# Performance work log

Hardware: AMD Instinct MI355X
Metric: run time of the kernel (lower is better)

The kernel has to match this reference:

```python
import jax, jax.numpy as jnp
import numpy as np

N_NODES, N_EDGES, N_GRAPHS = 50000, 800000, 512
F_IN, HID, DIM_OUT = 128, 256, 16


def setup_inputs() -> dict:
    key = jax.random.key(0)
    ks = jax.random.split(key, 16)
    glorot = lambda k, fi, fo: jax.random.normal(k, (fi, fo), jnp.float32) * jnp.sqrt(2.0 / (fi + fo))
    return {
        "x": jax.random.normal(ks[0], (N_NODES, F_IN), jnp.float32),
        "edge_index": jax.random.randint(ks[1], (2, N_EDGES), 0, N_NODES, dtype=jnp.int32),
        "batch": jnp.sort(jax.random.randint(ks[2], (N_NODES,), 0, N_GRAPHS, dtype=jnp.int32)),
        "mol_wt": jax.random.uniform(ks[3], (N_GRAPHS, 1), jnp.float32),
        "n_rings": jax.random.uniform(ks[4], (N_GRAPHS, 1), jnp.float32),
        "W1": glorot(ks[5], F_IN, HID), "b1": jnp.zeros((HID,), jnp.float32),
        "W2": glorot(ks[6], HID, HID), "b2": jnp.zeros((HID,), jnp.float32),
        "W3": glorot(ks[7], HID, HID), "b3": jnp.zeros((HID,), jnp.float32),
        "fcW1": glorot(ks[8], HID + 2, 196), "fcb1": jnp.zeros((196,), jnp.float32),
        "fcW2": glorot(ks[9], 196, DIM_OUT), "fcb2": jnp.zeros((DIM_OUT,), jnp.float32),
    }


def _gcn_conv(x, W, b, src, dst, deg_inv_sqrt, n_nodes):
    # PyG GCNConv: linear transform, then D^-1/2 (A+I) D^-1/2 aggregation, then bias
    xw = x @ W  # [N, HID]
    norm = deg_inv_sqrt[src] * deg_inv_sqrt[dst]  # [E+N]
    msg = norm[:, None] * xw[src]  # gather + scale
    out = jax.ops.segment_sum(msg, dst, num_segments=n_nodes)  # scatter-add at targets
    return out + b


def reference(x, edge_index, batch, mol_wt, n_rings,
              W1, b1, W2, b2, W3, b3, fcW1, fcb1, fcW2, fcb2):
    n_nodes = x.shape[0]
    self_loop = jnp.arange(n_nodes, dtype=edge_index.dtype)
    src = jnp.concatenate([edge_index[0], self_loop])
    dst = jnp.concatenate([edge_index[1], self_loop])
    deg = jax.ops.segment_sum(jnp.ones_like(dst, dtype=x.dtype), dst, num_segments=n_nodes)
    deg_inv_sqrt = jnp.where(deg > 0, jax.lax.rsqrt(deg), 0.0)

    h = jax.nn.relu(_gcn_conv(x, W1, b1, src, dst, deg_inv_sqrt, n_nodes))
    h = jax.nn.relu(_gcn_conv(h, W2, b2, src, dst, deg_inv_sqrt, n_nodes))
    h = jax.nn.relu(_gcn_conv(h, W3, b3, src, dst, deg_inv_sqrt, n_nodes))

    n_graphs = mol_wt.shape[0]
    sums = jax.ops.segment_sum(h, batch, num_segments=n_graphs)
    counts = jax.ops.segment_sum(jnp.ones((n_nodes,), h.dtype), batch, num_segments=n_graphs)
    hg = sums / jnp.maximum(counts, 1.0)[:, None]  # global mean pool

    hg = jnp.concatenate([hg, mol_wt, n_rings], axis=1)  # [G, 258]
    hg = jax.nn.relu(hg @ fcW1 + fcb1)
    return hg @ fcW2 + fcb2
```

## Files before the change

kernel.cpp:

```cpp
#include <hip/hip_runtime.h>

#define NN 50000
#define NE 800000
#define NG 512
#define FIN 128
#define HID 256
#define NBUK 196
#define SEGSZ 2048

typedef short short8 __attribute__((ext_vector_type(8)));
typedef float f32x4 __attribute__((ext_vector_type(4)));
typedef float f32x2 __attribute__((ext_vector_type(2)));
typedef unsigned short u16x8 __attribute__((ext_vector_type(8)));
typedef unsigned int u32x2 __attribute__((ext_vector_type(2)));
typedef unsigned int u32x4 __attribute__((ext_vector_type(4)));

static inline int cdiv(int a, int b) { return (a + b - 1) / b; }

static __device__ inline unsigned short f2bf(float f) {
    unsigned int u = __float_as_uint(f);
    unsigned int r = (u + 0x7FFF + ((u >> 16) & 1)) >> 16;
    return (unsigned short)r;
}
static __device__ inline float bf2f(unsigned short h) {
    return __uint_as_float(((unsigned int)h) << 16);
}
static __device__ inline float bflo(unsigned int p) { return __uint_as_float(p << 16); }
static __device__ inline float bfhi(unsigned int p) { return __uint_as_float(p & 0xFFFF0000u); }

static __device__ __forceinline__ f32x2 pkadd(f32x2 a, f32x2 b) {
    f32x2 r;
    asm("v_pk_add_f32 %0, %1, %2" : "=v"(r) : "v"(a), "v"(b));
    return r;
}

template <int J>
static __device__ __forceinline__ int bswz(int v) {
    return __builtin_amdgcn_ds_swizzle(v, (J << 5) | 0x18);
}

typedef __attribute__((address_space(1))) unsigned int gu32;
typedef __attribute__((address_space(3))) unsigned int lu32;
static __device__ __forceinline__ void gload16(const unsigned short* g, unsigned short* l) {
    __builtin_amdgcn_global_load_lds((const gu32*)(const void*)g, (lu32*)(void*)l, 16, 0, 0);
}


__global__ __launch_bounds__(256) void hist_bucket_kernel(const int* __restrict__ dst,
                                                          int* __restrict__ gbuk) {
    __shared__ int lh[NBUK];
    int tid = threadIdx.x;
    for (int j = tid; j < NBUK; j += 256) lh[j] = 0;
    __syncthreads();
    int base = blockIdx.x * 2048;
    #pragma unroll
    for (int k = 0; k < 8; ++k) {
        int i = base + k * 256 + tid;
        if (i < NE) atomicAdd(&lh[dst[i] >> 8], 1);
    }
    __syncthreads();
    for (int j = tid; j < NBUK; j += 256) if (lh[j]) atomicAdd(&gbuk[j], lh[j]);
}

__global__ void goff_kernel(const int* __restrict__ batch, int* __restrict__ goff) {
    int i = blockIdx.x * 256 + threadIdx.x;
    if (i >= NN) return;
    int b = batch[i];
    int pb = (i == 0) ? -1 : batch[i - 1];
    for (int g = pb + 1; g <= b; ++g) goff[g] = i;
    if (i == NN - 1) for (int g = b + 1; g <= NG; ++g) goff[g] = NN;
}

__global__ void buk_scan_kernel(const int* __restrict__ gbuk, int* __restrict__ bukoff,
                                int* __restrict__ bukcur) {
    __shared__ int ws[4];
    int tid = threadIdx.x, lane = tid & 63, wid = tid >> 6;
    int v = (tid < NBUK) ? gbuk[tid] : 0;
    int incl = v;
    #pragma unroll
    for (int off = 1; off < 64; off <<= 1) {
        int u = __shfl_up(incl, off, 64);
        if (lane >= off) incl += u;
    }
    if (lane == 63) ws[wid] = incl;
    __syncthreads();
    int woff = 0;
    for (int w = 0; w < wid; ++w) woff += ws[w];
    int ex = woff + incl - v;
    if (tid < NBUK) { bukoff[tid] = ex; bukcur[tid] = ex; }
    if (tid == NBUK - 1) bukoff[NBUK] = ex + v;
}

__global__ __launch_bounds__(256) void scatter_kernel(const int* __restrict__ src,
                                                      const int* __restrict__ dst,
                                                      int* __restrict__ bukcur,
                                                      unsigned int* __restrict__ pairs) {
    __shared__ int lh[NBUK];
    __shared__ int lbase[NBUK];
    int tid = threadIdx.x;
    for (int j = tid; j < NBUK; j += 256) lh[j] = 0;
    __syncthreads();
    int base = blockIdx.x * 2048;
    int d[8], s[8];
    #pragma unroll
    for (int k = 0; k < 8; ++k) {
        int i = base + k * 256 + tid;
        if (i < NE) {
            d[k] = dst[i]; s[k] = src[i];
            atomicAdd(&lh[d[k] >> 8], 1);
        } else d[k] = -1;
    }
    __syncthreads();
    for (int j = tid; j < NBUK; j += 256) lbase[j] = lh[j] ? atomicAdd(&bukcur[j], lh[j]) : 0;
    __syncthreads();
    for (int j = tid; j < NBUK; j += 256) lh[j] = 0;
    __syncthreads();
    #pragma unroll
    for (int k = 0; k < 8; ++k) {
        if (d[k] >= 0) {
            int b = d[k] >> 8;
            int loc = atomicAdd(&lh[b], 1);
            pairs[lbase[b] + loc] = ((unsigned int)s[k] << 16) | (unsigned int)(d[k] & 255);
        }
    }
}

__global__ __launch_bounds__(256) void local_csr_kernel(const unsigned int* __restrict__ pairs,
                                                        const int* __restrict__ bukoff,
                                                        int* __restrict__ row_ptr,
                                                        int* __restrict__ col8,
                                                        float* __restrict__ dis) {
    __shared__ int fcnt[256];
    __shared__ int foff[256];
    __shared__ int fws[4];
    int b = blockIdx.x, tid = threadIdx.x;
    int beg = bukoff[b], end = bukoff[b + 1];
    fcnt[tid] = 0;
    __syncthreads();
    for (int i = beg + tid; i < end; i += 256) atomicAdd(&fcnt[pairs[i] & 255], 1);
    __syncthreads();
    int lane = tid & 63, wid = tid >> 6;
    int v = fcnt[tid], incl = v;
    #pragma unroll
    for (int off = 1; off < 64; off <<= 1) {
        int u = __shfl_up(incl, off, 64);
        if (lane >= off) incl += u;
    }
    if (lane == 63) fws[wid] = incl;
    __syncthreads();
    int woff = 0;
    for (int w = 0; w < wid; ++w) woff += fws[w];
    int ex = woff + incl - v;
    foff[tid] = ex;
    int gid = b * 256 + tid;
    if (gid < NN) {
        row_ptr[gid] = beg + ex;
        dis[gid] = rsqrtf((float)v + 1.0f);
    }
    if (b == 0 && tid == 0) row_ptr[NN] = NE;
    __syncthreads();
    for (int i = beg + tid; i < end; i += 256) {
        unsigned int p = pairs[i];
        int loc = atomicAdd(&foff[p & 255], 1);
        col8[beg + loc] = (int)(p >> 16) << 3;
    }
}

__global__ __launch_bounds__(256) void segperm_kernel(const int* __restrict__ row_ptr,
                                                      const float* __restrict__ dis,
                                                      u32x4* __restrict__ desc) {
    __shared__ int hist[256];
    __shared__ int ws[4];
    int tid = threadIdx.x;
    int base = blockIdx.x * SEGSZ;
    int segN = NN - base; if (segN > SEGSZ) segN = SEGSZ;
    hist[tid] = 0;
    __syncthreads();
    int dbin[8], rb[8], dreal[8];
    #pragma unroll
    for (int k = 0; k < 8; ++k) {
        int j = k * 256 + tid;
        if (j < segN) {
            rb[k] = row_ptr[base + j];
            dreal[k] = row_ptr[base + j + 1] - rb[k];
            int d = dreal[k] > 255 ? 255 : dreal[k];
            dbin[k] = d;
            atomicAdd(&hist[d], 1);
        } else dbin[k] = -1;
    }
    __syncthreads();
    int lane = tid & 63, wid = tid >> 6;
    int v = hist[tid], incl = v;
    #pragma unroll
    for (int off = 1; off < 64; off <<= 1) {
        int u = __shfl_up(incl, off, 64);
        if (lane >= off) incl += u;
    }
    if (lane == 63) ws[wid] = incl;
    __syncthreads();
    int woff = 0;
    for (int w = 0; w < wid; ++w) woff += ws[w];
    __syncthreads();
    hist[tid] = woff + incl - v;
    __syncthreads();
    #pragma unroll
    for (int k = 0; k < 8; ++k) {
        if (dbin[k] >= 0) {
            int rank = atomicAdd(&hist[dbin[k]], 1);
            int node = base + k * 256 + tid;
            u32x4 dd;
            dd.x = (unsigned int)(node * 8);
            dd.y = (unsigned int)rb[k];
            dd.z = (unsigned int)(rb[k] + dreal[k]);
            dd.w = __float_as_uint(dis[node]);
            desc[base + rank] = dd;
        }
    }
}

__global__ void cast_scale_kernel(const float* __restrict__ x, const float* __restrict__ dis,
                                  unsigned short* __restrict__ Xb, int n4) {
    int i = blockIdx.x * 256 + threadIdx.x;
    if (i < n4) {
        int node = i >> 5;
        int f4 = i & 31;
        int s = f4 >> 3;
        int o = f4 & 7;
        float dv = dis[node];
        float4 v = ((const float4*)x)[i];
        ushort4 w;
        w.x = f2bf(dv * v.x); w.y = f2bf(dv * v.y); w.z = f2bf(dv * v.z); w.w = f2bf(dv * v.w);
        ((ushort4*)Xb)[((size_t)s * NN + (size_t)node) * 8 + o] = w;
    }
}

__global__ void tcast_all_kernel(const float* __restrict__ W1, const float* __restrict__ W2,
                                 const float* __restrict__ W3,
                                 unsigned short* __restrict__ W1t, unsigned short* __restrict__ W2t,
                                 unsigned short* __restrict__ W3t) {
    int idx = blockIdx.x * 256 + threadIdx.x;
    if (idx < FIN * 256) {
        int n = idx / FIN, k = idx - n * FIN;
        W1t[idx] = f2bf(W1[(size_t)k * 256 + n]);
    } else if (idx < FIN * 256 + HID * 256) {
        int t = idx - FIN * 256;
        int n = t / HID, k = t - n * HID;
        W2t[t] = f2bf(W2[(size_t)k * 256 + n]);
    } else {
        int t = idx - FIN * 256 - HID * 256;
        int n = t / HID, k = t - n * HID;
        W3t[t] = f2bf(W3[(size_t)k * 256 + n]);
    }
}

#define CLD 136
template <int MODE>
__global__ __launch_bounds__(256) void gemm128_kernel(
        const unsigned short* __restrict__ A, const unsigned short* __restrict__ Bt,
        const float* __restrict__ dis, const float* __restrict__ bias,
        unsigned short* __restrict__ Cout, int M, int K) {
    __shared__ unsigned short smem[128 * CLD];
    unsigned short* As = smem;
    unsigned short* Bs = smem + 4096;
    const int tid = threadIdx.x;
    const int bm = blockIdx.x * 128, bn = blockIdx.y * 128;
    const int wave = tid >> 6, lane = tid & 63;
    const int l16 = lane & 15, quad = lane >> 4;
    const int wm = (wave & 1) * 64, wn = (wave >> 1) * 64;

    int srow0 = tid >> 2, skc = (tid & 3) * 8;
    int srow1 = (256 + tid) >> 2;
    int ar0 = bm + srow0; if (ar0 > M - 1) ar0 = M - 1;
    int ar1 = bm + srow1; if (ar1 > M - 1) ar1 = M - 1;

    f32x4 acc[4][4];
    #pragma unroll
    for (int i = 0; i < 4; ++i)
        #pragma unroll
        for (int j = 0; j < 4; ++j) acc[i][j] = (f32x4){0.f, 0.f, 0.f, 0.f};

    for (int k0 = 0; k0 < K; k0 += 32) {
        gload16(A + (size_t)ar0 * K + k0 + skc, &As[(size_t)tid * 8]);
        gload16(A + (size_t)ar1 * K + k0 + skc, &As[(size_t)(256 + tid) * 8]);
        gload16(Bt + (size_t)(bn + srow0) * K + k0 + skc, &Bs[(size_t)tid * 8]);
        gload16(Bt + (size_t)(bn + srow1) * K + k0 + skc, &Bs[(size_t)(256 + tid) * 8]);
        __syncthreads();
        short8 af[4], bf[4];
        #pragma unroll
        for (int mt = 0; mt < 4; ++mt) af[mt] = *(const short8*)&As[(wm + mt * 16 + l16) * 32 + quad * 8];
        #pragma unroll
        for (int nt = 0; nt < 4; ++nt) bf[nt] = *(const short8*)&Bs[(wn + nt * 16 + l16) * 32 + quad * 8];
        #pragma unroll
        for (int mt = 0; mt < 4; ++mt)
            #pragma unroll
            for (int nt = 0; nt < 4; ++nt)
                acc[mt][nt] = __builtin_amdgcn_mfma_f32_16x16x32_bf16(af[mt], bf[nt], acc[mt][nt], 0, 0, 0);
        __syncthreads();
    }
    float bv[4];
    #pragma unroll
    for (int nt = 0; nt < 4; ++nt) bv[nt] = bias[bn + wn + nt * 16 + l16];
    #pragma unroll
    for (int mt = 0; mt < 4; ++mt) {
        #pragma unroll
        for (int r = 0; r < 4; ++r) {
            int lrow = wm + mt * 16 + quad * 4 + r;
            int grow = bm + lrow; if (grow > M - 1) grow = M - 1;
            float dv = (MODE == 0) ? dis[grow] : 1.0f;
            #pragma unroll
            for (int nt = 0; nt < 4; ++nt) {
                float v = fmaxf(acc[mt][nt][r] + bv[nt], 0.f);
                if (MODE == 0) v *= dv;
                smem[lrow * CLD + wn + nt * 16 + l16] = f2bf(v);
            }
        }
    }
    __syncthreads();
    for (int c = tid; c < 2048; c += 256) {
        int lrow = c >> 4, coff = (c & 15) << 3;
        int grow = bm + lrow;
        if (grow < M) {
            if (MODE == 0) {
                int gcol = bn + coff;
                int s = gcol >> 5, o = gcol & 31;
                *(u16x8*)(Cout + ((size_t)s * M + (size_t)grow) * 32 + o) =
                    *(const u16x8*)&smem[lrow * CLD + coff];
            } else {
                *(u16x8*)(Cout + (size_t)grow * HID + bn + coff) =
                    *(const u16x8*)&smem[lrow * CLD + coff];
            }
        }
    }
}
#undef CLD

template <int S>
__global__ __launch_bounds__(256) void agg_slice_kernel(
        const unsigned short* __restrict__ Hb, const u32x4* __restrict__ desc,
        const int* __restrict__ col8,
        unsigned short* __restrict__ Out, int n, int nchunk) {
    constexpr int LOGS = (S == 8) ? 3 : 2;
    int bid = blockIdx.x;
    int s = bid & (S - 1);
    int chunk = nchunk - 1 - (bid >> LOGS);
    int idx = chunk * 32 + (threadIdx.x >> 3);
    if (idx >= n) return;
    int lane8 = threadIdx.x & 7;
    u32x4 d = desc[idx];
    int node8 = (int)d.x;
    int e = (int)d.y, eend = (int)d.z;
    float dv = __uint_as_float(d.w);
    const u32x2* Hv = (const u32x2*)Hb + (size_t)s * NN * 8;
    u32x2 p = Hv[node8 + lane8];
    f32x2 a01 = {bflo(p.x), bfhi(p.x)};
    f32x2 a23 = {bflo(p.y), bfhi(p.y)};

    for (; e + 16 <= eend; e += 16) {
        int cv0 = col8[e + lane8];
        int cv1 = col8[e + 8 + lane8];
        u32x2 m[16];
#define G0(J) m[J] = Hv[bswz<J>(cv0) + lane8];
#define G1(J) m[8 + J] = Hv[bswz<J>(cv1) + lane8];
        G0(0) G0(1) G0(2) G0(3) G0(4) G0(5) G0(6) G0(7)
        G1(0) G1(1) G1(2) G1(3) G1(4) G1(5) G1(6) G1(7)
#undef G0
#undef G1
        #pragma unroll
        for (int j = 0; j < 16; ++j) {
            f32x2 lo = {bflo(m[j].x), bfhi(m[j].x)};
            f32x2 hi = {bflo(m[j].y), bfhi(m[j].y)};
            a01 = pkadd(a01, lo);
            a23 = pkadd(a23, hi);
        }
    }
    if (e + 8 <= eend) {
        int cv0 = col8[e + lane8];
        u32x2 m[8];
#define G0(J) m[J] = Hv[bswz<J>(cv0) + lane8];
        G0(0) G0(1) G0(2) G0(3) G0(4) G0(5) G0(6) G0(7)
#undef G0
        #pragma unroll
        for (int j = 0; j < 8; ++j) {
            f32x2 lo = {bflo(m[j].x), bfhi(m[j].x)};
            f32x2 hi = {bflo(m[j].y), bfhi(m[j].y)};
            a01 = pkadd(a01, lo);
            a23 = pkadd(a23, hi);
        }
        e += 8;
    }
    int t = eend - e;
    if (t > 0) {
        int il = e + lane8; if (il >= eend) il = eend - 1;
        int cv0 = col8[il];
        u32x2 m[7];
#define GT(J) if (J < t) m[J] = Hv[bswz<J>(cv0) + lane8];
        GT(0) GT(1) GT(2) GT(3) GT(4) GT(5) GT(6)
#undef GT
#define AT(J) if (J < t) { f32x2 lo = {bflo(m[J].x), bfhi(m[J].x)}; \
                           f32x2 hi = {bflo(m[J].y), bfhi(m[J].y)}; \
                           a01 = pkadd(a01, lo); a23 = pkadd(a23, hi); }
        AT(0) AT(1) AT(2) AT(3) AT(4) AT(5) AT(6)
#undef AT
    }
    int node = node8 >> 3;
    u32x2 o;
    o.x = (unsigned int)f2bf(dv * a01.x) | ((unsigned int)f2bf(dv * a01.y) << 16);
    o.y = (unsigned int)f2bf(dv * a23.x) | ((unsigned int)f2bf(dv * a23.y) << 16);
    __builtin_nontemporal_store(o, (u32x2*)Out + (size_t)node * (S * 8) + s * 8 + lane8);
}

__global__ __launch_bounds__(256) void pool_mlp_kernel(
        const unsigned short* __restrict__ H, const int* __restrict__ goff,
        const float* __restrict__ mol, const float* __restrict__ rings,
        const float* __restrict__ fcW1, const float* __restrict__ fcb1,
        const float* __restrict__ fcW2, const float* __restrict__ fcb2,
        float* __restrict__ out) {
    __shared__ float s_hg[258];
    __shared__ float s_t[196];
    int g = blockIdx.x, tid = threadIdx.x;
    int beg = goff[g], end = goff[g + 1];
    float acc = 0.f;
    for (int i = beg; i < end; ++i) acc += bf2f(H[(size_t)i * HID + tid]);
    s_hg[tid] = acc / fmaxf((float)(end - beg), 1.0f);
    if (tid == 0) { s_hg[256] = mol[g]; s_hg[257] = rings[g]; }
    __syncthreads();
    if (tid < 196) {
        float a = fcb1[tid];
        for (int k = 0; k < 258; ++k) a = fmaf(s_hg[k], fcW1[k * 196 + tid], a);
        s_t[tid] = fmaxf(a, 0.f);
    }
    __syncthreads();
    if (tid < 16) {
        float a = fcb2[tid];
        for (int k = 0; k < 196; ++k) a = fmaf(s_t[k], fcW2[k * 16 + tid], a);
        out[g * 16 + tid] = a;
    }
}

extern "C" void kernel_launch(void* const* d_in, const int* in_sizes, int n_in,
                              void* d_out, int out_size, void* d_ws, size_t ws_size,
                              hipStream_t stream) {
    const float* x     = (const float*)d_in[0];
    const int*   ei    = (const int*)d_in[1];
    const int*   batch = (const int*)d_in[2];
    const float* mol   = (const float*)d_in[3];
    const float* rings = (const float*)d_in[4];
    const float* W1 = (const float*)d_in[5];
    const float* b1 = (const float*)d_in[6];
    const float* W2 = (const float*)d_in[7];
    const float* b2 = (const float*)d_in[8];
    const float* W3 = (const float*)d_in[9];
    const float* b3 = (const float*)d_in[10];
    const float* fcW1 = (const float*)d_in[11];
    const float* fcb1 = (const float*)d_in[12];
    const float* fcW2 = (const float*)d_in[13];
    const float* fcb2 = (const float*)d_in[14];
    float* out = (float*)d_out;
    const int* src = ei;
    const int* dst = ei + NE;

    char* w = (char*)d_ws;
    auto alloc = [&](size_t bytes) {
        char* p = w;
        w += (bytes + 255) & ~(size_t)255;
        return p;
    };
    int*   gbuk    = (int*)alloc((size_t)NBUK * 4);
    int*   bukoff  = (int*)alloc((size_t)(NBUK + 1) * 4);
    int*   bukcur  = (int*)alloc((size_t)NBUK * 4);
    int*   row_ptr = (int*)alloc((size_t)(NN + 1) * 4);
    int*   goff    = (int*)alloc((size_t)(NG + 1) * 4);
    float* dis     = (float*)alloc((size_t)NN * 4);
    u32x4* desc    = (u32x4*)alloc((size_t)NN * 16);
    unsigned int* pairs = (unsigned int*)alloc((size_t)NE * 4);
    int*   col8    = (int*)alloc((size_t)NE * 4);
    unsigned short* Xs  = (unsigned short*)alloc((size_t)NN * FIN * 2);
    unsigned short* Xa  = (unsigned short*)alloc((size_t)NN * FIN * 2);
    unsigned short* Hs  = (unsigned short*)alloc((size_t)NN * HID * 2);
    unsigned short* Ga  = (unsigned short*)alloc((size_t)NN * HID * 2);
    unsigned short* Hf  = (unsigned short*)alloc((size_t)NN * HID * 2);
    unsigned short* W1t = (unsigned short*)alloc((size_t)FIN * HID * 2);
    unsigned short* W2t = (unsigned short*)alloc((size_t)HID * HID * 2);
    unsigned short* W3t = (unsigned short*)alloc((size_t)HID * HID * 2);

    hipMemsetAsync(gbuk, 0, (size_t)NBUK * 4, stream);
    int eb = cdiv(NE, 2048);
    hist_bucket_kernel<<<eb, 256, 0, stream>>>(dst, gbuk);
    goff_kernel<<<cdiv(NN, 256), 256, 0, stream>>>(batch, goff);
    buk_scan_kernel<<<1, 256, 0, stream>>>(gbuk, bukoff, bukcur);
    scatter_kernel<<<eb, 256, 0, stream>>>(src, dst, bukcur, pairs);
    local_csr_kernel<<<NBUK, 256, 0, stream>>>(pairs, bukoff, row_ptr, col8, dis);
    segperm_kernel<<<cdiv(NN, SEGSZ), 256, 0, stream>>>(row_ptr, dis, desc);

    cast_scale_kernel<<<cdiv(NN * FIN / 4, 256), 256, 0, stream>>>(x, dis, Xs, NN * FIN / 4);
    tcast_all_kernel<<<cdiv((FIN + HID + HID) * 256, 256), 256, 0, stream>>>(W1, W2, W3, W1t, W2t, W3t);

    dim3 ggrid(cdiv(NN, 128), 2);
    int achunks = cdiv(NN, 32);
    agg_slice_kernel<4><<<4 * achunks, 256, 0, stream>>>(Xs, desc, col8, Xa, NN, achunks);
    gemm128_kernel<0><<<ggrid, 256, 0, stream>>>(Xa, W1t, dis, b1, Hs, NN, FIN);
    agg_slice_kernel<8><<<8 * achunks, 256, 0, stream>>>(Hs, desc, col8, Ga, NN, achunks);
    gemm128_kernel<0><<<ggrid, 256, 0, stream>>>(Ga, W2t, dis, b2, Hs, NN, HID);
    agg_slice_kernel<8><<<8 * achunks, 256, 0, stream>>>(Hs, desc, col8, Ga, NN, achunks);
    gemm128_kernel<1><<<ggrid, 256, 0, stream>>>(Ga, W3t, dis, b3, Hf, NN, HID);
    pool_mlp_kernel<<<NG, 256, 0, stream>>>(Hf, goff, mol, rings, fcW1, fcb1, fcW2, fcb2, out);
}
```

Baseline: 365.6 us.

## Split mean-pool into parallel partial-sum kernel and separate MLP kernel

Graph mean pooling moves out of the MLP kernel into a new kernel. It launches four blocks per graph, and each thread reads four bf16 features per row across several rows at once, with a shared-memory reduction at the end. The MLP kernel then sums the four partials, unrolls the fcW1 dot-product loads, and splits the second layer across all 256 threads. This targets the serial per-graph row loop that left the final kernel latency-bound, at the cost of an extra launch and a small workspace round-trip.

After: 351.3 us. 1.04x faster.

```diff
diff --git a/kernel.cpp b/kernel.cpp
--- a/kernel.cpp
+++ b/kernel.cpp
@@ -409,30 +409,94 @@
     __builtin_nontemporal_store(o, (u32x2*)Out + (size_t)node * (S * 8) + s * 8 + lane8);
 }
 
-__global__ __launch_bounds__(256) void pool_mlp_kernel(
+__global__ __launch_bounds__(256) void pool_part_kernel(
         const unsigned short* __restrict__ H, const int* __restrict__ goff,
+        float* __restrict__ part) {
+    __shared__ float red[3][64][4];
+    int bid = blockIdx.x;
+    int g = bid >> 2, q = bid & 3;
+    int beg = goff[g], end = goff[g + 1];
+    int len = end - beg;
+    int qb = beg + ((len * q) >> 2), qe = beg + ((len * (q + 1)) >> 2);
+    int tp = threadIdx.x >> 6, tf = threadIdx.x & 63;
+    float4 acc = make_float4(0.f, 0.f, 0.f, 0.f);
+    int i = qb + tp;
+    for (; i + 12 < qe; i += 16) {
+        ushort4 v0 = *(const ushort4*)&H[(size_t)(i     ) * HID + tf * 4];
+        ushort4 v1 = *(const ushort4*)&H[(size_t)(i +  4) * HID + tf * 4];
+        ushort4 v2 = *(const ushort4*)&H[(size_t)(i +  8) * HID + tf * 4];
+        ushort4 v3 = *(const ushort4*)&H[(size_t)(i + 12) * HID + tf * 4];
+        acc.x += bf2f(v0.x) + bf2f(v1.x) + bf2f(v2.x) + bf2f(v3.x);
+        acc.y += bf2f(v0.y) + bf2f(v1.y) + bf2f(v2.y) + bf2f(v3.y);
+        acc.z += bf2f(v0.z) + bf2f(v1.z) + bf2f(v2.z) + bf2f(v3.z);
+        acc.w += bf2f(v0.w) + bf2f(v1.w) + bf2f(v2.w) + bf2f(v3.w);
+    }
+    for (; i < qe; i += 4) {
+        ushort4 v = *(const ushort4*)&H[(size_t)i * HID + tf * 4];
+        acc.x += bf2f(v.x); acc.y += bf2f(v.y); acc.z += bf2f(v.z); acc.w += bf2f(v.w);
+    }
+    if (tp > 0) {
+        red[tp - 1][tf][0] = acc.x; red[tp - 1][tf][1] = acc.y;
+        red[tp - 1][tf][2] = acc.z; red[tp - 1][tf][3] = acc.w;
+    }
+    __syncthreads();
+    if (tp == 0) {
+        acc.x += red[0][tf][0] + red[1][tf][0] + red[2][tf][0];
+        acc.y += red[0][tf][1] + red[1][tf][1] + red[2][tf][1];
+        acc.z += red[0][tf][2] + red[1][tf][2] + red[2][tf][2];
+        acc.w += red[0][tf][3] + red[1][tf][3] + red[2][tf][3];
+        ((float4*)part)[(size_t)bid * 64 + tf] = acc;
+    }
+}
+
+__global__ __launch_bounds__(256) void mlp_kernel(
+        const float* __restrict__ part, const int* __restrict__ goff,
         const float* __restrict__ mol, const float* __restrict__ rings,
         const float* __restrict__ fcW1, const float* __restrict__ fcb1,
         const float* __restrict__ fcW2, const float* __restrict__ fcb2,
         float* __restrict__ out) {
     __shared__ float s_hg[258];
     __shared__ float s_t[196];
+    __shared__ float s_p[16][16];
     int g = blockIdx.x, tid = threadIdx.x;
-    int beg = goff[g], end = goff[g + 1];
-    float acc = 0.f;
-    for (int i = beg; i < end; ++i) acc += bf2f(H[(size_t)i * HID + tid]);
-    s_hg[tid] = acc / fmaxf((float)(end - beg), 1.0f);
+    int len = goff[g + 1] - goff[g];
+    const float* pg = part + (size_t)g * 1024;
+    float v = pg[tid] + pg[256 + tid] + pg[512 + tid] + pg[768 + tid];
+    s_hg[tid] = v / fmaxf((float)len, 1.0f);
     if (tid == 0) { s_hg[256] = mol[g]; s_hg[257] = rings[g]; }
     __syncthreads();
     if (tid < 196) {
         float a = fcb1[tid];
-        for (int k = 0; k < 258; ++k) a = fmaf(s_hg[k], fcW1[k * 196 + tid], a);
+        int k = 0;
+        for (; k + 8 <= 258; k += 8) {
+            float w0 = fcW1[(k + 0) * 196 + tid];
+            float w1 = fcW1[(k + 1) * 196 + tid];
+            float w2 = fcW1[(k + 2) * 196 + tid];
+            float w3 = fcW1[(k + 3) * 196 + tid];
+            float w4 = fcW1[(k + 4) * 196 + tid];
+            float w5 = fcW1[(k + 5) * 196 + tid];
+            float w6 = fcW1[(k + 6) * 196 + tid];
+            float w7 = fcW1[(k + 7) * 196 + tid];
+            a = fmaf(s_hg[k + 0], w0, a); a = fmaf(s_hg[k + 1], w1, a);
+            a = fmaf(s_hg[k + 2], w2, a); a = fmaf(s_hg[k + 3], w3, a);
+            a = fmaf(s_hg[k + 4], w4, a); a = fmaf(s_hg[k + 5], w5, a);
+            a = fmaf(s_hg[k + 6], w6, a); a = fmaf(s_hg[k + 7], w7, a);
+        }
+        for (; k < 258; ++k) a = fmaf(s_hg[k], fcW1[k * 196 + tid], a);
         s_t[tid] = fmaxf(a, 0.f);
+    }
+    __syncthreads();
+    {
+        int o = tid & 15, kp = tid >> 4;
+        float a = 0.f;
+        for (int k = kp; k < 196; k += 16) a = fmaf(s_t[k], fcW2[k * 16 + o], a);
+        s_p[kp][o] = a;
     }
     __syncthreads();
     if (tid < 16) {
         float a = fcb2[tid];
-        for (int k = 0; k < 196; ++k) a = fmaf(s_t[k], fcW2[k * 16 + tid], a);
+        #pragma unroll
+        for (int kp = 0; kp < 16; ++kp) a += s_p[kp][tid];
         out[g * 16 + tid] = a;
     }
 }
@@ -474,6 +538,7 @@
     u32x4* desc    = (u32x4*)alloc((size_t)NN * 16);
     unsigned int* pairs = (unsigned int*)alloc((size_t)NE * 4);
     int*   col8    = (int*)alloc((size_t)NE * 4);
+    float* part    = (float*)alloc((size_t)NG * 4 * 256 * 4);
     unsigned short* Xs  = (unsigned short*)alloc((size_t)NN * FIN * 2);
     unsigned short* Xa  = (unsigned short*)alloc((size_t)NN * FIN * 2);
     unsigned short* Hs  = (unsigned short*)alloc((size_t)NN * HID * 2);
@@ -503,5 +568,6 @@
     gemm128_kernel<0><<<ggrid, 256, 0, stream>>>(Ga, W2t, dis, b2, Hs, NN, HID);
     agg_slice_kernel<8><<<8 * achunks, 256, 0, stream>>>(Hs, desc, col8, Ga, NN, achunks);
     gemm128_kernel<1><<<ggrid, 256, 0, stream>>>(Ga, W3t, dis, b3, Hf, NN, HID);
-    pool_mlp_kernel<<<NG, 256, 0, stream>>>(Hf, goff, mol, rings, fcW1, fcb1, fcW2, fcb2, out);
-}
+    pool_part_kernel<<<NG * 4, 256, 0, stream>>>(Hf, goff, part);
+    mlp_kernel<<<NG, 256, 0, stream>>>(part, goff, mol, rings, fcW1, fcb1, fcW2, fcb2, out);
+}
```
